# Kernel tuning notes

Measured on AMD Instinct MI355X. Metric: run time of the kernel, lower is better.

Reference implementation:

```python
import jax, jax.numpy as jnp
import numpy as np
from jax import lax

C_IN, C_KEY, C_VAL = 1024, 256, 512

def conv3x3(x, w, b):
    # x: [B,C_in,H,W], w: [C_out,C_in,3,3] -> SAME padding, stride 1
    y = lax.conv_general_dilated(x, w, window_strides=(1, 1), padding='SAME',
                                 dimension_numbers=('NCHW', 'OIHW', 'NCHW'))
    return y + b[None, :, None, None]

def setup_inputs() -> dict:
    key = jax.random.key(0)
    ks = jax.random.split(key, 10)
    B, H, W = 16, 32, 32
    conv_std = 0.01  # matches torch init.normal_(std=0.01)
    inp = {
        'src_temp': jax.random.normal(ks[0], (B, C_IN, H, W), jnp.float32),
        'src_search': jax.random.normal(ks[1], (B, C_IN, H, W), jnp.float32),
        'wk_m': jax.random.normal(ks[2], (C_KEY, C_IN, 3, 3), jnp.float32) * conv_std,
        'bk_m': jnp.zeros((C_KEY,), jnp.float32),
        'wv_m': jax.random.normal(ks[3], (C_VAL, C_IN, 3, 3), jnp.float32) * conv_std,
        'bv_m': jnp.zeros((C_VAL,), jnp.float32),
        'wk_q': jax.random.normal(ks[4], (C_KEY, C_IN, 3, 3), jnp.float32) * conv_std,
        'bk_q': jnp.zeros((C_KEY,), jnp.float32),
        'wv_q': jax.random.normal(ks[5], (C_VAL, C_IN, 3, 3), jnp.float32) * conv_std,
        'bv_q': jnp.zeros((C_VAL,), jnp.float32),
    }
    return inp

def reference(src_temp, src_search, wk_m, bk_m, wv_m, bv_m, wk_q, bk_q, wv_q, bv_q):
    # key/value projections
    m_key = conv3x3(src_temp, wk_m, bk_m)      # [B, Ck, H, W]
    m_value = conv3x3(src_temp, wv_m, bv_m)    # [B, Cv, H, W]
    q_key = conv3x3(src_search, wk_q, bk_q)    # [B, Ck, H, W]
    q_value = conv3x3(src_search, wv_q, bv_q)  # [B, Cv, H, W]

    B, Ck, H, W = m_key.shape
    Cv = m_value.shape[1]
    HW = H * W

    mk = m_key.reshape(B, Ck, HW)   # [B, Ck, HW_m]
    qk = q_key.reshape(B, Ck, HW)   # [B, Ck, HW_q]
    # scores: [B, HW_m, HW_q]
    w = jnp.einsum('bcm,bcq->bmq', mk, qk) / jnp.sqrt(jnp.float32(Ck))
    w = jax.nn.softmax(w, axis=1)   # normalize over memory locations

    mv = m_value.reshape(B, Cv, HW)            # [B, Cv, HW_m]
    mem_info = jnp.einsum('bcm,bmq->bcq', mv, w).reshape(B, Cv, H, W)
    return jnp.concatenate([mem_info, q_value], axis=1)  # [B, 2*Cv, H, W]
```

## Files before the change

### kernel.cpp

```cpp
#include <hip/hip_runtime.h>
#include <stdint.h>

typedef __bf16 bf16;
typedef __bf16 bf16x8 __attribute__((ext_vector_type(8)));
typedef float  f32x4  __attribute__((ext_vector_type(4)));
typedef unsigned int u32;

#define OFF_AHI   0ull
#define OFF_ALO   18939904ull
#define OFF_WHI   37879808ull
#define OFF_WLO   52035584ull
#define OFF_QKEYT 67108864ull
#define OFF_MKEYT 83886080ull
#define OFF_MVAL  100663296ull
#define OFF_WATTN 0ull

__device__ __forceinline__ void split(float v, bf16& h, bf16& l) {
    h = (bf16)v;
    l = (bf16)(v - (float)h);
}

__device__ __forceinline__ u32 packsplit(float v) {
    bf16 h = (bf16)v;
    bf16 l = (bf16)(v - (float)h);
    unsigned short hu = __builtin_bit_cast(unsigned short, h);
    unsigned short lu = __builtin_bit_cast(unsigned short, l);
    return (u32)hu | ((u32)lu << 16);
}

__device__ __forceinline__ void deint4(const uint4 v, uint2& h, uint2& l) {
    h.x = (v.x & 0xffffu) | (v.y << 16);
    h.y = (v.z & 0xffffu) | (v.w << 16);
    l.x = (v.x >> 16) | (v.y & 0xffff0000u);
    l.y = (v.z >> 16) | (v.w & 0xffff0000u);
}

__global__ __launch_bounds__(256) void k_wt(const float* __restrict__ wk,
                                            const float* __restrict__ wv,
                                            bf16* __restrict__ Wh, bf16* __restrict__ Wl) {
    size_t id = (size_t)blockIdx.x * 256 + threadIdx.x;
    int e = (int)(id & 7);
    size_t t = id >> 3;
    int mm = (int)(t % 96); t /= 96;
    int coff = (int)(t & 3); t >>= 2;
    int cch = (int)(t & 31); t >>= 5;
    int r = (int)(t % 9);
    int mt = (int)(t / 9);
    int m = mt * 96 + mm;
    int c = cch * 32 + coff * 8 + e;
    float v = (m < 256) ? wk[((size_t)m * 1024 + c) * 9 + r]
                        : wv[((size_t)(m - 256) * 1024 + c) * 9 + r];
    bf16 h, l;
    split(v, h, l);
    Wh[id] = h; Wl[id] = l;
}

__global__ __launch_bounds__(256) void k_zero(bf16* __restrict__ Ah, bf16* __restrict__ Al) {
    int id = blockIdx.x * 256 + threadIdx.x;
    int oct = id & 127;
    int t = id >> 7;
    int pos = t % 132; t /= 132;
    int bl = t & 7, hl = t >> 3;
    int yy, xx;
    if (pos < 34)       { yy = 0;  xx = pos; }
    else if (pos < 68)  { yy = 33; xx = pos - 34; }
    else if (pos < 100) { yy = pos - 68 + 1;  xx = 0; }
    else                { yy = pos - 100 + 1; xx = 33; }
    bf16* base = hl ? Al : Ah;
    size_t off = (((size_t)bl * 34 + yy) * 34 + xx) * 1024 + (size_t)oct * 8;
    *(uint4*)(base + off) = make_uint4(0u, 0u, 0u, 0u);
}

__global__ __launch_bounds__(256) void k_transpose(const float* __restrict__ src,
                                                   bf16* __restrict__ Ah, bf16* __restrict__ Al) {
    int pt = blockIdx.x, ct = blockIdx.y, bl = blockIdx.z;
    __shared__ float tile[64][68];
    int t = threadIdx.x;
    #pragma unroll
    for (int k = 0; k < 4; ++k) {
        int idx = t + 256 * k;
        int c = idx >> 4, f4 = idx & 15;
        float4 v = *(const float4*)(src + ((size_t)bl * 1024 + ct * 64 + c) * 1024 + pt * 64 + f4 * 4);
        *(float4*)&tile[c][f4 * 4] = v;
    }
    __syncthreads();
    #pragma unroll
    for (int k = 0; k < 2; ++k) {
        int s = t + 256 * k;
        int px = s >> 3, oct = s & 7;
        bf16x8 vh, vl;
        #pragma unroll
        for (int e = 0; e < 8; ++e) {
            bf16 h, l;
            split(tile[oct * 8 + e][px], h, l);
            vh[e] = h; vl[e] = l;
        }
        int pxg = pt * 64 + px;
        int yy = (pxg >> 5) + 1, xx = (pxg & 31) + 1;
        size_t off = (((size_t)bl * 34 + yy) * 34 + xx) * 1024 + ct * 64 + oct * 8;
        *(bf16x8*)(Ah + off) = vh;
        *(bf16x8*)(Al + off) = vl;
    }
}

#define XS_STRIDE 40
__global__ __launch_bounds__(256) void k_conv(const bf16* __restrict__ Ah, const bf16* __restrict__ Al,
                                              const bf16* __restrict__ Wh, const bf16* __restrict__ Wl,
                                              const float* __restrict__ biask, const float* __restrict__ biasv,
                                              u32* __restrict__ keyT, float* __restrict__ valf,
                                              u32* __restrict__ valp, int bglob) {
    int bl = blockIdx.x >> 3, rg = blockIdx.x & 7;
    int mt = blockIdx.y;
    int y0 = rg * 4;
    int b = bglob + bl;

    __shared__ bf16 Xs[2 * 6 * 34 * XS_STRIDE];

    int tid = threadIdx.x;
    int w = tid >> 6, l = tid & 63;
    int wm = (w & 1) * 48, wn = (w >> 1) * 64;
    int lm = l & 15, lq = l >> 4;
    int koff = lq * 8;

    f32x4 acc[3][4] = {};

    const size_t Abase = ((size_t)bl * 34 + y0) * 34 * 1024;
    const size_t wlane = (size_t)lq * 768 + (size_t)lm * 8;

    for (int cch = 0; cch < 32; ++cch) {
        int c0 = cch * 32;
        bf16x8 xv[7];
        int lidx[7];
        #pragma unroll
        for (int it = 0; it < 7; ++it) {
            int s = tid + 256 * it;
            if (s < 1632) {
                int hl = s >= 816;
                int r816 = s - hl * 816;
                int row = r816 / 136;
                int rr = r816 - row * 136;
                int px = rr >> 2, oct = rr & 3;
                const bf16* base = hl ? Al : Ah;
                xv[it] = *(const bf16x8*)(base + Abase + ((size_t)row * 34 + px) * 1024 + c0 + oct * 8);
                lidx[it] = ((hl * 6 + row) * 34 + px) * XS_STRIDE + oct * 8;
            } else lidx[it] = -1;
        }
        __syncthreads();
        #pragma unroll
        for (int it = 0; it < 7; ++it)
            if (lidx[it] >= 0) *(bf16x8*)&Xs[lidx[it]] = xv[it];
        __syncthreads();

        #pragma unroll
        for (int r = 0; r < 9; ++r) {
            int dy = r / 3, dx = r % 3;
            size_t wblk = (((size_t)mt * 9 + r) * 32 + cch) * 3072 + wlane;
            bf16x8 ah[3], al[3];
            #pragma unroll
            for (int i = 0; i < 3; ++i) {
                size_t o = wblk + (size_t)(wm + i * 16) * 8;
                ah[i] = *(const bf16x8*)(Wh + o);
                al[i] = *(const bf16x8*)(Wl + o);
            }
            #pragma unroll
            for (int j = 0; j < 4; ++j) {
                int n = wn + j * 16 + lm;
                int lbase = (((n >> 5) + dy) * 34 + (n & 31) + dx) * XS_STRIDE + koff;
                bf16x8 bh = *(const bf16x8*)&Xs[lbase];
                bf16x8 blo = *(const bf16x8*)&Xs[6 * 34 * XS_STRIDE + lbase];
                #pragma unroll
                for (int i = 0; i < 3; ++i) {
                    acc[i][j] = __builtin_amdgcn_mfma_f32_16x16x32_bf16(ah[i], bh,  acc[i][j], 0, 0, 0);
                    acc[i][j] = __builtin_amdgcn_mfma_f32_16x16x32_bf16(ah[i], blo, acc[i][j], 0, 0, 0);
                    acc[i][j] = __builtin_amdgcn_mfma_f32_16x16x32_bf16(al[i], bh,  acc[i][j], 0, 0, 0);
                }
            }
        }
    }

    int col = lm, rowb = lq * 4;
    #pragma unroll
    for (int i = 0; i < 3; ++i) {
        int ch4 = mt * 96 + wm + i * 16 + rowb;
        #pragma unroll
        for (int j = 0; j < 4; ++j) {
            int px = rg * 128 + wn + j * 16 + col;
            if (ch4 < 256) {
                u32 p0 = packsplit(acc[i][j][0] + biask[ch4 + 0]);
                u32 p1 = packsplit(acc[i][j][1] + biask[ch4 + 1]);
                u32 p2 = packsplit(acc[i][j][2] + biask[ch4 + 2]);
                u32 p3 = packsplit(acc[i][j][3] + biask[ch4 + 3]);
                *(uint4*)(keyT + ((size_t)b * 1024 + px) * 256 + ch4) = make_uint4(p0, p1, p2, p3);
            } else {
                int cv = ch4 - 256;
                if (valp) {
                    #pragma unroll
                    for (int e = 0; e < 4; ++e)
                        valp[((size_t)b * 512 + cv + e) * 1024 + px] = packsplit(acc[i][j][e] + biasv[cv + e]);
                } else {
                    #pragma unroll
                    for (int e = 0; e < 4; ++e)
                        valf[((size_t)b * 1024 + 512 + cv + e) * 1024 + px] = acc[i][j][e] + biasv[cv + e];
                }
            }
        }
    }
}

#define AS 40
__global__ __launch_bounds__(256) void k_scores(const u32* __restrict__ qkT,
                                                const u32* __restrict__ mkT,
                                                float* __restrict__ wattn) {
    int mt = blockIdx.x, qt = blockIdx.y, b = blockIdx.z;
    __shared__ bf16 Qh[128][AS], Ql[128][AS], Mh[128][AS], Ml[128][AS];
    int t = threadIdx.x;
    int w_ = t >> 6, l = t & 63;
    int wq = (w_ & 1) * 64, wm = (w_ >> 1) * 64;
    int lm = l & 15, lq = l >> 4, koff = lq * 8;
    int srow = t >> 1, sc4 = (t & 1) * 16;
    const u32* qbase = qkT + ((size_t)b * 1024 + qt * 128 + srow) * 256 + sc4;
    const u32* mbase = mkT + ((size_t)b * 1024 + mt * 128 + srow) * 256 + sc4;
    f32x4 acc[4][4] = {};
    uint4 qv[4], mv[4];
    #pragma unroll
    for (int k = 0; k < 4; ++k) { qv[k] = *(const uint4*)(qbase + k * 4); mv[k] = *(const uint4*)(mbase + k * 4); }
    for (int cc = 0; cc < 8; ++cc) {
        __syncthreads();
        #pragma unroll
        for (int k = 0; k < 4; ++k) {
            uint2 h, lo;
            deint4(qv[k], h, lo);
            *(uint2*)&Qh[srow][sc4 + k * 4] = h;
            *(uint2*)&Ql[srow][sc4 + k * 4] = lo;
            deint4(mv[k], h, lo);
            *(uint2*)&Mh[srow][sc4 + k * 4] = h;
            *(uint2*)&Ml[srow][sc4 + k * 4] = lo;
        }
        __syncthreads();
        if (cc < 7) {
            #pragma unroll
            for (int k = 0; k < 4; ++k) {
                qv[k] = *(const uint4*)(qbase + (cc + 1) * 32 + k * 4);
                mv[k] = *(const uint4*)(mbase + (cc + 1) * 32 + k * 4);
            }
        }
        bf16x8 ah[4], al[4];
        #pragma unroll
        for (int iq = 0; iq < 4; ++iq) {
            ah[iq] = *(const bf16x8*)&Qh[wq + iq * 16 + lm][koff];
            al[iq] = *(const bf16x8*)&Ql[wq + iq * 16 + lm][koff];
        }
        #pragma unroll
        for (int jm = 0; jm < 4; ++jm) {
            bf16x8 bh = *(const bf16x8*)&Mh[wm + jm * 16 + lm][koff];
            bf16x8 bl = *(const bf16x8*)&Ml[wm + jm * 16 + lm][koff];
            #pragma unroll
            for (int iq = 0; iq < 4; ++iq) {
                acc[iq][jm] = __builtin_amdgcn_mfma_f32_16x16x32_bf16(ah[iq], bh, acc[iq][jm], 0, 0, 0);
                acc[iq][jm] = __builtin_amdgcn_mfma_f32_16x16x32_bf16(ah[iq], bl, acc[iq][jm], 0, 0, 0);
                acc[iq][jm] = __builtin_amdgcn_mfma_f32_16x16x32_bf16(al[iq], bh, acc[iq][jm], 0, 0, 0);
            }
        }
    }
    #pragma unroll
    for (int iq = 0; iq < 4; ++iq) {
        int q = qt * 128 + wq + iq * 16 + lq * 4;
        #pragma unroll
        for (int jm = 0; jm < 4; ++jm) {
            int m = mt * 128 + wm + jm * 16 + lm;
            float* wp = wattn + ((size_t)b * 1024 + q) * 1024 + m;
            #pragma unroll
            for (int e = 0; e < 4; ++e)
                wp[(size_t)e * 1024] = acc[iq][jm][e] * 0.0625f;
        }
    }
}

__global__ __launch_bounds__(256) void k_softmax(float* __restrict__ wattn) {
    int row = blockIdx.x * 4 + (threadIdx.x >> 6);
    int l = threadIdx.x & 63;
    float* base = wattn + (size_t)row * 1024;
    float4 v[4];
    #pragma unroll
    for (int k = 0; k < 4; ++k) v[k] = *(float4*)(base + l * 4 + k * 256);
    float f[16];
    #pragma unroll
    for (int k = 0; k < 4; ++k) { f[4*k]=v[k].x; f[4*k+1]=v[k].y; f[4*k+2]=v[k].z; f[4*k+3]=v[k].w; }
    float mx = -3.0e38f;
    #pragma unroll
    for (int e = 0; e < 16; ++e) mx = fmaxf(mx, f[e]);
    #pragma unroll
    for (int off = 32; off > 0; off >>= 1) mx = fmaxf(mx, __shfl_xor(mx, off));
    float s = 0.0f;
    #pragma unroll
    for (int e = 0; e < 16; ++e) { f[e] = __expf(f[e] - mx); s += f[e]; }
    #pragma unroll
    for (int off = 32; off > 0; off >>= 1) s += __shfl_xor(s, off);
    float inv = 1.0f / s;
    u32* ub = (u32*)base;
    #pragma unroll
    for (int k = 0; k < 4; ++k) {
        uint4 u = make_uint4(packsplit(f[4*k]   * inv), packsplit(f[4*k+1] * inv),
                             packsplit(f[4*k+2] * inv), packsplit(f[4*k+3] * inv));
        *(uint4*)(ub + l * 4 + k * 256) = u;
    }
}

__global__ __launch_bounds__(256) void k_memv(const u32* __restrict__ mvalp,
                                              const u32* __restrict__ wattnp,
                                              float* __restrict__ outp) {
    int ct = blockIdx.x, qt = blockIdx.y, b = blockIdx.z;
    __shared__ bf16 Vh[128][AS], Vl[128][AS], Wh[128][AS], Wl[128][AS];
    int t = threadIdx.x;
    int w_ = t >> 6, l = t & 63;
    int wc = (w_ & 1) * 64, wq = (w_ >> 1) * 64;
    int lm = l & 15, lq = l >> 4, koff = lq * 8;
    int srow = t >> 1, sc4 = (t & 1) * 16;
    const u32* vbase = mvalp  + ((size_t)b * 512  + ct * 128 + srow) * 1024 + sc4;
    const u32* wbase = wattnp + ((size_t)b * 1024 + qt * 128 + srow) * 1024 + sc4;
    f32x4 acc[4][4] = {};
    uint4 vv[4], wv[4];
    #pragma unroll
    for (int k = 0; k < 4; ++k) { vv[k] = *(const uint4*)(vbase + k * 4); wv[k] = *(const uint4*)(wbase + k * 4); }
    for (int mc = 0; mc < 32; ++mc) {
        __syncthreads();
        #pragma unroll
        for (int k = 0; k < 4; ++k) {
            uint2 h, lo;
            deint4(vv[k], h, lo);
            *(uint2*)&Vh[srow][sc4 + k * 4] = h;
            *(uint2*)&Vl[srow][sc4 + k * 4] = lo;
            deint4(wv[k], h, lo);
            *(uint2*)&Wh[srow][sc4 + k * 4] = h;
            *(uint2*)&Wl[srow][sc4 + k * 4] = lo;
        }
        __syncthreads();
        if (mc < 31) {
            #pragma unroll
            for (int k = 0; k < 4; ++k) {
                vv[k] = *(const uint4*)(vbase + (mc + 1) * 32 + k * 4);
                wv[k] = *(const uint4*)(wbase + (mc + 1) * 32 + k * 4);
            }
        }
        bf16x8 ah[4], al[4];
        #pragma unroll
        for (int ic = 0; ic < 4; ++ic) {
            ah[ic] = *(const bf16x8*)&Vh[wc + ic * 16 + lm][koff];
            al[ic] = *(const bf16x8*)&Vl[wc + ic * 16 + lm][koff];
        }
        #pragma unroll
        for (int jq = 0; jq < 4; ++jq) {
            bf16x8 bh = *(const bf16x8*)&Wh[wq + jq * 16 + lm][koff];
            bf16x8 bl = *(const bf16x8*)&Wl[wq + jq * 16 + lm][koff];
            #pragma unroll
            for (int ic = 0; ic < 4; ++ic) {
                acc[ic][jq] = __builtin_amdgcn_mfma_f32_16x16x32_bf16(ah[ic], bh, acc[ic][jq], 0, 0, 0);
                acc[ic][jq] = __builtin_amdgcn_mfma_f32_16x16x32_bf16(ah[ic], bl, acc[ic][jq], 0, 0, 0);
                acc[ic][jq] = __builtin_amdgcn_mfma_f32_16x16x32_bf16(al[ic], bh, acc[ic][jq], 0, 0, 0);
            }
        }
    }
    #pragma unroll
    for (int ic = 0; ic < 4; ++ic) {
        int c = ct * 128 + wc + ic * 16 + lq * 4;
        #pragma unroll
        for (int jq = 0; jq < 4; ++jq) {
            int q = qt * 128 + wq + jq * 16 + lm;
            #pragma unroll
            for (int e = 0; e < 4; ++e)
                outp[((size_t)b * 1024 + c + e) * 1024 + q] = acc[ic][jq][e];
        }
    }
}

extern "C" void kernel_launch(void* const* d_in, const int* in_sizes, int n_in,
                              void* d_out, int out_size, void* d_ws, size_t ws_size,
                              hipStream_t stream) {
    const float* src_temp   = (const float*)d_in[0];
    const float* src_search = (const float*)d_in[1];
    const float* wk_m = (const float*)d_in[2];
    const float* bk_m = (const float*)d_in[3];
    const float* wv_m = (const float*)d_in[4];
    const float* bv_m = (const float*)d_in[5];
    const float* wk_q = (const float*)d_in[6];
    const float* bk_q = (const float*)d_in[7];
    const float* wv_q = (const float*)d_in[8];
    const float* bv_q = (const float*)d_in[9];
    float* out = (float*)d_out;
    char* ws = (char*)d_ws;
    bf16* Ah = (bf16*)(ws + OFF_AHI);
    bf16* Al = (bf16*)(ws + OFF_ALO);
    bf16* Wh = (bf16*)(ws + OFF_WHI);
    bf16* Wl = (bf16*)(ws + OFF_WLO);
    u32* qkP = (u32*)(ws + OFF_QKEYT);
    u32* mkP = (u32*)(ws + OFF_MKEYT);
    u32* mvP = (u32*)(ws + OFF_MVAL);
    float* wattn = (float*)(ws + OFF_WATTN);
    u32* wattnP = (u32*)(ws + OFF_WATTN);

    hipLaunchKernelGGL(k_zero, dim3(1056), dim3(256), 0, stream, Ah, Al);

    hipLaunchKernelGGL(k_wt, dim3(27648), dim3(256), 0, stream, wk_q, wv_q, Wh, Wl);
    for (int h = 0; h < 2; ++h) {
        hipLaunchKernelGGL(k_transpose, dim3(16, 16, 8), dim3(256), 0, stream,
                           src_search + (size_t)h * 8 * 1024 * 1024, Ah, Al);
        hipLaunchKernelGGL(k_conv, dim3(64, 8), dim3(256), 0, stream,
                           Ah, Al, Wh, Wl, bk_q, bv_q, qkP, out, (u32*)nullptr, h * 8);
    }
    hipLaunchKernelGGL(k_wt, dim3(27648), dim3(256), 0, stream, wk_m, wv_m, Wh, Wl);
    for (int h = 0; h < 2; ++h) {
        hipLaunchKernelGGL(k_transpose, dim3(16, 16, 8), dim3(256), 0, stream,
                           src_temp + (size_t)h * 8 * 1024 * 1024, Ah, Al);
        hipLaunchKernelGGL(k_conv, dim3(64, 8), dim3(256), 0, stream,
                           Ah, Al, Wh, Wl, bk_m, bv_m, mkP, (float*)nullptr, mvP, h * 8);
    }

    hipLaunchKernelGGL(k_scores,  dim3(8, 8, 16), dim3(256), 0, stream, qkP, mkP, wattn);
    hipLaunchKernelGGL(k_softmax, dim3(4096),     dim3(256), 0, stream, wattn);
    hipLaunchKernelGGL(k_memv,    dim3(4, 8, 16), dim3(256), 0, stream, mvP, wattnP, out);
}
```

Baseline: 1.591 ms.

## Double-buffer conv input tile in LDS and prefetch next channel chunk

The conv kernel now keeps two LDS buffers for the activation tile. It issues the global loads for the next 32-channel chunk before the MFMA work on the current chunk and writes them to the other buffer afterwards, which cuts the barriers per iteration from two to one and hides global-load latency. Address computation is hoisted out of the loop, and launch bounds ask for 2 blocks per CU. In exchange, LDS use doubles and prefetched registers stay live, which may limit occupancy or cause spills.

```diff
diff --git a/kernel.cpp b/kernel.cpp
--- a/kernel.cpp
+++ b/kernel.cpp
@@ -104,17 +104,18 @@
 }
 
 #define XS_STRIDE 40
-__global__ __launch_bounds__(256) void k_conv(const bf16* __restrict__ Ah, const bf16* __restrict__ Al,
-                                              const bf16* __restrict__ Wh, const bf16* __restrict__ Wl,
-                                              const float* __restrict__ biask, const float* __restrict__ biasv,
-                                              u32* __restrict__ keyT, float* __restrict__ valf,
-                                              u32* __restrict__ valp, int bglob) {
+#define XS_HALF   (6 * 34 * XS_STRIDE)
+__global__ __launch_bounds__(256, 2) void k_conv(const bf16* __restrict__ Ah, const bf16* __restrict__ Al,
+                                                 const bf16* __restrict__ Wh, const bf16* __restrict__ Wl,
+                                                 const float* __restrict__ biask, const float* __restrict__ biasv,
+                                                 u32* __restrict__ keyT, float* __restrict__ valf,
+                                                 u32* __restrict__ valp, int bglob) {
     int bl = blockIdx.x >> 3, rg = blockIdx.x & 7;
     int mt = blockIdx.y;
     int y0 = rg * 4;
     int b = bglob + bl;
 
-    __shared__ bf16 Xs[2 * 6 * 34 * XS_STRIDE];
+    __shared__ bf16 Xs[2][2 * XS_HALF];
 
     int tid = threadIdx.x;
     int w = tid >> 6, l = tid & 63;
@@ -127,29 +128,43 @@
     const size_t Abase = ((size_t)bl * 34 + y0) * 34 * 1024;
     const size_t wlane = (size_t)lq * 768 + (size_t)lm * 8;
 
+    const bf16* gsrc[7];
+    int lidx[7];
+    #pragma unroll
+    for (int it = 0; it < 7; ++it) {
+        int s = tid + 256 * it;
+        if (s < 1632) {
+            int hl = s >= 816;
+            int r816 = s - hl * 816;
+            int row = r816 / 136;
+            int rr = r816 - row * 136;
+            int px = rr >> 2, oct = rr & 3;
+            const bf16* base = hl ? Al : Ah;
+            gsrc[it] = base + Abase + ((size_t)row * 34 + px) * 1024 + oct * 8;
+            lidx[it] = ((hl * 6 + row) * 34 + px) * XS_STRIDE + oct * 8;
+        } else { gsrc[it] = nullptr; lidx[it] = -1; }
+    }
+
+    {
+        bf16x8 xv[7];
+        #pragma unroll
+        for (int it = 0; it < 7; ++it)
+            if (lidx[it] >= 0) xv[it] = *(const bf16x8*)(gsrc[it]);
+        #pragma unroll
+        for (int it = 0; it < 7; ++it)
+            if (lidx[it] >= 0) *(bf16x8*)&Xs[0][lidx[it]] = xv[it];
+    }
+    __syncthreads();
+
     for (int cch = 0; cch < 32; ++cch) {
-        int c0 = cch * 32;
-        bf16x8 xv[7];
-        int lidx[7];
-        #pragma unroll
-        for (int it = 0; it < 7; ++it) {
-            int s = tid + 256 * it;
-            if (s < 1632) {
-                int hl = s >= 816;
-                int r816 = s - hl * 816;
-                int row = r816 / 136;
-                int rr = r816 - row * 136;
-                int px = rr >> 2, oct = rr & 3;
-                const bf16* base = hl ? Al : Ah;
-                xv[it] = *(const bf16x8*)(base + Abase + ((size_t)row * 34 + px) * 1024 + c0 + oct * 8);
-                lidx[it] = ((hl * 6 + row) * 34 + px) * XS_STRIDE + oct * 8;
-            } else lidx[it] = -1;
-        }
-        __syncthreads();
-        #pragma unroll
-        for (int it = 0; it < 7; ++it)
-            if (lidx[it] >= 0) *(bf16x8*)&Xs[lidx[it]] = xv[it];
-        __syncthreads();
+        int cur = cch & 1;
+        bf16x8 xn[7];
+        if (cch < 31) {
+            int c0n = (cch + 1) * 32;
+            #pragma unroll
+            for (int it = 0; it < 7; ++it)
+                if (lidx[it] >= 0) xn[it] = *(const bf16x8*)(gsrc[it] + c0n);
+        }
 
         #pragma unroll
         for (int r = 0; r < 9; ++r) {
@@ -166,8 +181,8 @@
             for (int j = 0; j < 4; ++j) {
                 int n = wn + j * 16 + lm;
                 int lbase = (((n >> 5) + dy) * 34 + (n & 31) + dx) * XS_STRIDE + koff;
-                bf16x8 bh = *(const bf16x8*)&Xs[lbase];
-                bf16x8 blo = *(const bf16x8*)&Xs[6 * 34 * XS_STRIDE + lbase];
+                bf16x8 bh  = *(const bf16x8*)&Xs[cur][lbase];
+                bf16x8 blo = *(const bf16x8*)&Xs[cur][XS_HALF + lbase];
                 #pragma unroll
                 for (int i = 0; i < 3; ++i) {
                     acc[i][j] = __builtin_amdgcn_mfma_f32_16x16x32_bf16(ah[i], bh,  acc[i][j], 0, 0, 0);
@@ -175,6 +190,13 @@
                     acc[i][j] = __builtin_amdgcn_mfma_f32_16x16x32_bf16(al[i], bh,  acc[i][j], 0, 0, 0);
                 }
             }
+        }
+
+        if (cch < 31) {
+            #pragma unroll
+            for (int it = 0; it < 7; ++it)
+                if (lidx[it] >= 0) *(bf16x8*)&Xs[cur ^ 1][lidx[it]] = xn[it];
+            __syncthreads();
         }
     }
 
```

New measurement: 1.630 ms. 2.5% more time.

## Split conv K-loop across two thread halves with LDS reduction

Applied to the files above, without the earlier changes.

Each conv block now runs 512 threads: two groups of four waves, each handling half of the input-channel chunks with its own LDS tile. At the end one group writes its accumulators to LDS and the other adds them before the epilogue. This doubles the waves per block so the MFMA/load latency of the 512-block grid is hidden better. The cost is more LDS per block, a reduction pass, and a register cap from the new launch bounds.

```diff
diff --git a/kernel.cpp b/kernel.cpp
--- a/kernel.cpp
+++ b/kernel.cpp
@@ -104,20 +104,23 @@
 }
 
 #define XS_STRIDE 40
-__global__ __launch_bounds__(256) void k_conv(const bf16* __restrict__ Ah, const bf16* __restrict__ Al,
-                                              const bf16* __restrict__ Wh, const bf16* __restrict__ Wl,
-                                              const float* __restrict__ biask, const float* __restrict__ biasv,
-                                              u32* __restrict__ keyT, float* __restrict__ valf,
-                                              u32* __restrict__ valp, int bglob) {
+#define XS_HALF   (6 * 34 * XS_STRIDE)
+__global__ __launch_bounds__(512, 4) void k_conv(const bf16* __restrict__ Ah, const bf16* __restrict__ Al,
+                                                 const bf16* __restrict__ Wh, const bf16* __restrict__ Wl,
+                                                 const float* __restrict__ biask, const float* __restrict__ biasv,
+                                                 u32* __restrict__ keyT, float* __restrict__ valf,
+                                                 u32* __restrict__ valp, int bglob) {
     int bl = blockIdx.x >> 3, rg = blockIdx.x & 7;
     int mt = blockIdx.y;
     int y0 = rg * 4;
     int b = bglob + bl;
 
-    __shared__ bf16 Xs[2 * 6 * 34 * XS_STRIDE];
+    __shared__ bf16 Xs[2][2 * XS_HALF];
 
     int tid = threadIdx.x;
-    int w = tid >> 6, l = tid & 63;
+    int half = tid >> 8;
+    int t256 = tid & 255;
+    int w = t256 >> 6, l = t256 & 63;
     int wm = (w & 1) * 48, wn = (w >> 1) * 64;
     int lm = l & 15, lq = l >> 4;
     int koff = lq * 8;
@@ -127,13 +130,14 @@
     const size_t Abase = ((size_t)bl * 34 + y0) * 34 * 1024;
     const size_t wlane = (size_t)lq * 768 + (size_t)lm * 8;
 
-    for (int cch = 0; cch < 32; ++cch) {
+    for (int ii = 0; ii < 16; ++ii) {
+        int cch = half * 16 + ii;
         int c0 = cch * 32;
         bf16x8 xv[7];
         int lidx[7];
         #pragma unroll
         for (int it = 0; it < 7; ++it) {
-            int s = tid + 256 * it;
+            int s = t256 + 256 * it;
             if (s < 1632) {
                 int hl = s >= 816;
                 int r816 = s - hl * 816;
@@ -148,7 +152,7 @@
         __syncthreads();
         #pragma unroll
         for (int it = 0; it < 7; ++it)
-            if (lidx[it] >= 0) *(bf16x8*)&Xs[lidx[it]] = xv[it];
+            if (lidx[it] >= 0) *(bf16x8*)&Xs[half][lidx[it]] = xv[it];
         __syncthreads();
 
         #pragma unroll
@@ -166,8 +170,8 @@
             for (int j = 0; j < 4; ++j) {
                 int n = wn + j * 16 + lm;
                 int lbase = (((n >> 5) + dy) * 34 + (n & 31) + dx) * XS_STRIDE + koff;
-                bf16x8 bh = *(const bf16x8*)&Xs[lbase];
-                bf16x8 blo = *(const bf16x8*)&Xs[6 * 34 * XS_STRIDE + lbase];
+                bf16x8 bh  = *(const bf16x8*)&Xs[half][lbase];
+                bf16x8 blo = *(const bf16x8*)&Xs[half][XS_HALF + lbase];
                 #pragma unroll
                 for (int i = 0; i < 3; ++i) {
                     acc[i][j] = __builtin_amdgcn_mfma_f32_16x16x32_bf16(ah[i], bh,  acc[i][j], 0, 0, 0);
@@ -177,6 +181,24 @@
             }
         }
     }
+
+    __syncthreads();
+    float* red = (float*)&Xs[0][0];
+    if (half) {
+        #pragma unroll
+        for (int i = 0; i < 3; ++i)
+            #pragma unroll
+            for (int j = 0; j < 4; ++j)
+                *(f32x4*)&red[((size_t)t256 * 12 + i * 4 + j) * 4] = acc[i][j];
+    }
+    __syncthreads();
+    if (half) return;
+
+    #pragma unroll
+    for (int i = 0; i < 3; ++i)
+        #pragma unroll
+        for (int j = 0; j < 4; ++j)
+            acc[i][j] += *(const f32x4*)&red[((size_t)t256 * 12 + i * 4 + j) * 4];
 
     int col = lm, rowb = lq * 4;
     #pragma unroll
@@ -404,14 +426,14 @@
     for (int h = 0; h < 2; ++h) {
         hipLaunchKernelGGL(k_transpose, dim3(16, 16, 8), dim3(256), 0, stream,
                            src_search + (size_t)h * 8 * 1024 * 1024, Ah, Al);
-        hipLaunchKernelGGL(k_conv, dim3(64, 8), dim3(256), 0, stream,
+        hipLaunchKernelGGL(k_conv, dim3(64, 8), dim3(512), 0, stream,
                            Ah, Al, Wh, Wl, bk_q, bv_q, qkP, out, (u32*)nullptr, h * 8);
     }
     hipLaunchKernelGGL(k_wt, dim3(27648), dim3(256), 0, stream, wk_m, wv_m, Wh, Wl);
     for (int h = 0; h < 2; ++h) {
         hipLaunchKernelGGL(k_transpose, dim3(16, 16, 8), dim3(256), 0, stream,
                            src_temp + (size_t)h * 8 * 1024 * 1024, Ah, Al);
-        hipLaunchKernelGGL(k_conv, dim3(64, 8), dim3(256), 0, stream,
+        hipLaunchKernelGGL(k_conv, dim3(64, 8), dim3(512), 0, stream,
                            Ah, Al, Wh, Wl, bk_m, bv_m, mkP, (float*)nullptr, mvP, h * 8);
     }
 
```

Result: slower. 2.042 ms (+28.3%).
